# Kernel optimization log

Hardware: AMD Instinct MI355X
Metric: run time of the kernel (lower is better)

The kernel has to match this reference:

```python
import jax, jax.numpy as jnp
import numpy as np

S = 32          # input grid resolution
N = 2048        # active input voxels
C = 256         # in channels
CO = 128        # out channels
S2 = 2 * S      # upsampled resolution
M = 8 * N       # candidate child voxels
EPS = 1e-6


def setup_inputs() -> dict:
    key = jax.random.key(0)
    ks = jax.random.split(key, 8)
    # unique voxel coordinates (sparse occupancy)
    lin = jax.random.permutation(ks[0], S ** 3)[:N]
    coords = jnp.stack([lin // (S * S), (lin // S) % S, lin % S], axis=-1).astype(jnp.int32)
    sc = 0.05
    return {
        "feats": jax.random.normal(ks[1], (N, C), jnp.float32),
        "norm1_w": 1.0 + 0.1 * jax.random.normal(ks[2], (C,), jnp.float32),
        "norm1_b": 0.1 * jax.random.normal(ks[3], (C,), jnp.float32),
        "subdiv_w": sc * jax.random.normal(ks[4], (C, 8), jnp.float32),
        "subdiv_b": jnp.zeros((8,), jnp.float32),
        "conv1_w": sc * jax.random.normal(ks[5], (27, C, CO), jnp.float32),
        "conv1_b": jnp.zeros((CO,), jnp.float32),
        "conv2_w": sc * jax.random.normal(ks[6], (27, CO, CO), jnp.float32),
        "conv2_b": jnp.zeros((CO,), jnp.float32),
        "skip_w": sc * jax.random.normal(ks[7], (C, CO), jnp.float32),
        "skip_b": jnp.zeros((CO,), jnp.float32),
        "coords": coords,
    }


def _layernorm(x, w=None, b=None):
    # LayerNorm32: fp32 math, eps=1e-6
    m = jnp.mean(x, axis=-1, keepdims=True)
    v = jnp.var(x, axis=-1, keepdims=True)
    y = (x - m) * jax.lax.rsqrt(v + EPS)
    if w is not None:
        y = y * w + b
    return y


def _sparse_conv(feats, nidx, w, b):
    # submanifold 3x3x3 sparse conv: gather 27 neighbors, contract.
    # nidx: [M,27] with sentinel M pointing at a zero row.
    pad = jnp.concatenate([feats, jnp.zeros((1, feats.shape[1]), feats.dtype)], axis=0)
    g = pad[nidx]                                   # [M, 27, Cin]
    return jnp.einsum('nkc,kcd->nd', g, w) + b


def _forward(feats, norm1_w, norm1_b, subdiv_w, subdiv_b, conv1_w, conv1_b,
             conv2_w, conv2_b, skip_w, skip_b, coords):
    # subdiv prediction (SparseLinear C -> 8)
    subdiv = feats @ subdiv_w + subdiv_b            # [N, 8]
    # norm1 + silu
    h = jax.nn.silu(_layernorm(feats, norm1_w, norm1_b))
    # sparse upsample x2 with octree subdivision mask
    mask = (subdiv > 0).reshape(-1)                 # [M]
    j = jnp.arange(8, dtype=jnp.int32)
    offs8 = jnp.stack([(j >> 2) & 1, (j >> 1) & 1, j & 1], axis=-1)  # [8,3]
    cc = (coords[:, None, :] * 2 + offs8[None]).reshape(-1, 3)        # [M,3]
    h_c = jnp.where(mask[:, None], jnp.repeat(h, 8, axis=0), 0.0)     # [M,C]
    x_c = jnp.where(mask[:, None], jnp.repeat(feats, 8, axis=0), 0.0)
    # neighbor lookup grid (padded by 1; default M -> zero feature row)
    grid = jnp.full((S2 + 2, S2 + 2, S2 + 2), M, jnp.int32)
    grid = grid.at[cc[:, 0] + 1, cc[:, 1] + 1, cc[:, 2] + 1].set(
        jnp.arange(M, dtype=jnp.int32))
    d = jnp.arange(-1, 2, dtype=jnp.int32)
    offs27 = jnp.stack(jnp.meshgrid(d, d, d, indexing='ij'), axis=-1).reshape(27, 3)
    nc = cc[:, None, :] + 1 + offs27[None]          # [M,27,3]
    nidx = grid[nc[..., 0], nc[..., 1], nc[..., 2]] # [M,27]
    # conv1 -> norm2 (no affine) -> silu -> conv2
    h1 = jax.nn.silu(_layernorm(_sparse_conv(h_c, nidx, conv1_w, conv1_b)))
    h2 = _sparse_conv(h1, nidx, conv2_w, conv2_b)
    # residual with linear skip; mask out non-subdivided children
    out = (h2 + x_c @ skip_w + skip_b) * mask[:, None].astype(h2.dtype)
    return out, subdiv


def reference(feats, norm1_w, norm1_b, subdiv_w, subdiv_b, conv1_w, conv1_b,
              conv2_w, conv2_b, skip_w, skip_b, coords):
    return _forward(feats, norm1_w, norm1_b, subdiv_w, subdiv_b, conv1_w,
                    conv1_b, conv2_w, conv2_b, skip_w, skip_b, coords)
```

## Files before the change

kernel.cpp:

```cpp
#include <hip/hip_runtime.h>
#include <cstdint>
#include <cstddef>

constexpr int N  = 2048;
constexpr int C  = 256;
constexpr int CO = 128;
constexpr int M  = 16384;
constexpr int G  = 66;
constexpr int KP = 7;
constexpr int KCHUNK = 4;
constexpr float EPS = 1e-6f;

using bf8 = __attribute__((ext_vector_type(8))) short;
using f4  = __attribute__((ext_vector_type(4))) float;

#define AS1 __attribute__((address_space(1)))
#define AS3 __attribute__((address_space(3)))

static __device__ __forceinline__ void gl_lds16(const void* g, void* l) {
  __builtin_amdgcn_global_load_lds((AS1 const void*)g, (AS3 void*)l, 16, 0, 0);
}

static __device__ __forceinline__ unsigned short f2bf(float f) {
  unsigned u = __float_as_uint(f);
  u += 0x7fffu + ((u >> 16) & 1u);
  return (unsigned short)(u >> 16);
}

__global__ void k_init(int* __restrict__ grid, unsigned short* __restrict__ h,
                       unsigned short* __restrict__ h1) {
  int i = blockIdx.x * 256 + threadIdx.x;
  if (i < G * G * G) grid[i] = M;
  if (i < C)  h[(size_t)N * C + i] = 0;
  if (i < CO) h1[(size_t)M * CO + i] = 0;
}

template <int CIN>
__global__ void k_wt(const float* __restrict__ w, unsigned short* __restrict__ wt) {
  int i = blockIdx.x * 256 + threadIdx.x;
  if (i >= 27 * CIN * CO) return;
  int c = i % CIN;
  int rest = i / CIN;
  int o = rest % CO;
  int k = rest / CO;
  wt[i] = f2bf(w[((size_t)(k * CIN + c)) * CO + o]);
}

__global__ __launch_bounds__(256) void k_rownorm(
    const float* __restrict__ feats, const float* __restrict__ n1w,
    const float* __restrict__ n1b, const float* __restrict__ sdw,
    const float* __restrict__ sdb, float* __restrict__ out_subdiv,
    unsigned short* __restrict__ h, int* __restrict__ pidx,
    float* __restrict__ maskf) {
  int n = blockIdx.x, t = threadIdx.x;
  float x = feats[(size_t)n * C + t];
  float4 w0 = *(const float4*)(sdw + t * 8);
  float4 w1 = *(const float4*)(sdw + t * 8 + 4);
  float v[10] = {x * w0.x, x * w0.y, x * w0.z, x * w0.w,
                 x * w1.x, x * w1.y, x * w1.z, x * w1.w, x, x * x};
#pragma unroll
  for (int mk = 1; mk < 64; mk <<= 1) {
#pragma unroll
    for (int j = 0; j < 10; ++j) v[j] += __shfl_xor(v[j], mk, 64);
  }
  __shared__ float red[4][10];
  int wave = t >> 6, lane = t & 63;
  if (lane == 0) {
#pragma unroll
    for (int j = 0; j < 10; ++j) red[wave][j] = v[j];
  }
  __syncthreads();
  float sums[10];
#pragma unroll
  for (int j = 0; j < 10; ++j)
    sums[j] = red[0][j] + red[1][j] + red[2][j] + red[3][j];
  float mean = sums[8] / (float)C;
  float var  = sums[9] / (float)C - mean * mean;
  float rstd = rsqrtf(var + EPS);
  if (t < 8) {
    float sd = sums[t] + sdb[t];
    out_subdiv[(size_t)n * 8 + t] = sd;
    bool mk = sd > 0.f;
    pidx[n * 8 + t]  = mk ? n : N;
    maskf[n * 8 + t] = mk ? 1.f : 0.f;
  }
  float y  = (x - mean) * rstd * n1w[t] + n1b[t];
  float sl = y / (1.f + __expf(-y));
  h[(size_t)n * C + t] = f2bf(sl);
}

__global__ void k_scatter(const int* __restrict__ coords, int* __restrict__ grid) {
  int m = blockIdx.x * 256 + threadIdx.x;
  if (m >= M) return;
  int p = m >> 3, j = m & 7;
  int x = coords[p * 3 + 0] * 2 + ((j >> 2) & 1) + 1;
  int y = coords[p * 3 + 1] * 2 + ((j >> 1) & 1) + 1;
  int z = coords[p * 3 + 2] * 2 + (j & 1) + 1;
  grid[(x * G + y) * G + z] = m;
}

__global__ void k_nidx(const int* __restrict__ coords, const int* __restrict__ grid,
                       const int* __restrict__ pidx, int* __restrict__ nidxt,
                       int* __restrict__ g1t) {
  int idx = blockIdx.x * 256 + threadIdx.x;
  if (idx >= M * 27) return;
  int m = idx & (M - 1);
  int k = idx >> 14;
  int p = m >> 3, j = m & 7;
  int dx = k / 9 - 1;
  int dy = (k / 3) % 3 - 1;
  int dz = k % 3 - 1;
  int x = coords[p * 3 + 0] * 2 + ((j >> 2) & 1) + 1 + dx;
  int y = coords[p * 3 + 1] * 2 + ((j >> 1) & 1) + 1 + dy;
  int z = coords[p * 3 + 2] * 2 + (j & 1) + 1 + dz;
  int gv = grid[(x * G + y) * G + z];
  nidxt[idx] = gv;
  g1t[idx] = (gv == M) ? N : pidx[gv];
}

__global__ __launch_bounds__(256) void k_skip(const float* __restrict__ feats,
                                              const float* __restrict__ skw,
                                              const float* __restrict__ skb,
                                              float* __restrict__ s) {
  __shared__ float tile[32][36];
  int t = threadIdx.x;
  int rb = (blockIdx.x >> 1) * 32;
  int ob = (blockIdx.x & 1) * 64;
  int o = ob + (t & 63);
  int rg = (t >> 6) * 8;
  float acc[8] = {0, 0, 0, 0, 0, 0, 0, 0};
  for (int cb = 0; cb < C; cb += 32) {
    __syncthreads();
    int row = t >> 3, cc = (t & 7) * 4;
    *(float4*)&tile[row][cc] =
        *(const float4*)(feats + (size_t)(rb + row) * C + cb + cc);
    __syncthreads();
    for (int c = 0; c < 32; ++c) {
      float wv = skw[(size_t)(cb + c) * CO + o];
#pragma unroll
      for (int r = 0; r < 8; ++r) acc[r] += tile[rg + r][c] * wv;
    }
  }
  float bv = skb[o];
#pragma unroll
  for (int r = 0; r < 8; ++r) s[(size_t)(rb + rg + r) * CO + o] = acc[r] + bv;
}

template <int CIN, int NCB>
__global__ __launch_bounds__(256, 4) void k_conv(
    const unsigned short* __restrict__ src, const int* __restrict__ gt,
    const unsigned short* __restrict__ wt, float* __restrict__ part) {
  __shared__ unsigned short sA[2][128 * 32];
  __shared__ unsigned short sB[2][128 * 32];
  const int t = threadIdx.x;
  const int w = t >> 6, lane = t & 63;
  const int quad = lane >> 4, ln = lane & 15;
  const int m0 = blockIdx.x * 128;
  const int kpart = blockIdx.y;
  const int k0 = kpart * KCHUNK;
  const int nk = min(KCHUNK, 27 - k0);
  const int nstage = nk * NCB;
  const int rh = (w >> 1) * 64, ch = (w & 1) * 64;

  const int srow = lane >> 2;
  const int gchunk = (lane & 3) ^ ((lane >> 3) & 3);

  int ga[KCHUNK][2];
#pragma unroll
  for (int kk = 0; kk < KCHUNK; ++kk) {
#pragma unroll
    for (int rr = 0; rr < 2; ++rr) {
      ga[kk][rr] = (kk < nk)
          ? gt[(size_t)(k0 + kk) * M + m0 + rr * 64 + w * 16 + (lane >> 2)]
          : 0;
    }
  }
  (void)srow;

  auto stage = [&](int s, int buf) {
    const int kk = s / NCB;
    const int cb = s - kk * NCB;
    const int colbase = cb * 32 + gchunk * 8;
#pragma unroll
    for (int rr = 0; rr < 2; ++rr) {
      gl_lds16(src + (size_t)ga[kk][rr] * CIN + colbase,
               &sA[buf][(rr * 64 + w * 16) * 32]);
    }
#pragma unroll
    for (int rr = 0; rr < 2; ++rr) {
      const int corow = rr * 64 + w * 16 + (lane >> 2);
      gl_lds16(wt + ((size_t)(k0 + kk) * CO + corow) * CIN + colbase,
               &sB[buf][(rr * 64 + w * 16) * 32]);
    }
  };

  f4 acc[16];
  f4 zero = {0.f, 0.f, 0.f, 0.f};
#pragma unroll
  for (int i = 0; i < 16; ++i) acc[i] = zero;

  const int slot = quad ^ ((ln >> 1) & 3);

  stage(0, 0);
  for (int s = 0; s < nstage; ++s) {
    __syncthreads();
    if (s + 1 < nstage) stage(s + 1, (s + 1) & 1);
    const unsigned short* pa = sA[s & 1];
    const unsigned short* pb = sB[s & 1];
    bf8 av[4], bv[4];
#pragma unroll
    for (int ti = 0; ti < 4; ++ti) {
      int row = rh + ti * 16 + ln;
      av[ti] = *(const bf8*)(pa + row * 32 + slot * 8);
    }
#pragma unroll
    for (int tj = 0; tj < 4; ++tj) {
      int row = ch + tj * 16 + ln;
      bv[tj] = *(const bf8*)(pb + row * 32 + slot * 8);
    }
#pragma unroll
    for (int ti = 0; ti < 4; ++ti)
#pragma unroll
      for (int tj = 0; tj < 4; ++tj)
        acc[ti * 4 + tj] = __builtin_amdgcn_mfma_f32_16x16x32_bf16(
            av[ti], bv[tj], acc[ti * 4 + tj], 0, 0, 0);
  }

  float* pp = part + ((size_t)kpart * M + m0) * CO;
#pragma unroll
  for (int ti = 0; ti < 4; ++ti) {
    int mrow = rh + ti * 16 + quad * 4;
#pragma unroll
    for (int tj = 0; tj < 4; ++tj) {
      int co = ch + tj * 16 + ln;
#pragma unroll
      for (int rr = 0; rr < 4; ++rr)
        pp[(size_t)(mrow + rr) * CO + co] = acc[ti * 4 + tj][rr];
    }
  }
}

__global__ __launch_bounds__(256) void k_r1(const float* __restrict__ p,
                                            const float* __restrict__ bias,
                                            unsigned short* __restrict__ h1) {
  int wave = threadIdx.x >> 6, lane = threadIdx.x & 63;
  int m = blockIdx.x * 4 + wave;
  float v0 = bias[lane], v1 = bias[lane + 64];
#pragma unroll
  for (int q = 0; q < KP; ++q) {
    const float* pq = p + ((size_t)q * M + m) * CO;
    v0 += pq[lane];
    v1 += pq[lane + 64];
  }
  float sum = v0 + v1, sq = v0 * v0 + v1 * v1;
#pragma unroll
  for (int mk = 1; mk < 64; mk <<= 1) {
    sum += __shfl_xor(sum, mk, 64);
    sq  += __shfl_xor(sq, mk, 64);
  }
  float mean = sum / (float)CO;
  float var  = sq / (float)CO - mean * mean;
  float rstd = rsqrtf(var + EPS);
  float y0 = (v0 - mean) * rstd;
  float y1 = (v1 - mean) * rstd;
  float s0 = y0 / (1.f + __expf(-y0));
  float s1 = y1 / (1.f + __expf(-y1));
  h1[(size_t)m * CO + lane]      = f2bf(s0);
  h1[(size_t)m * CO + lane + 64] = f2bf(s1);
}

__global__ __launch_bounds__(256) void k_r2(const float* __restrict__ p,
                                            const float* __restrict__ bias,
                                            const float* __restrict__ sres,
                                            const float* __restrict__ maskf,
                                            float* __restrict__ out) {
  int i = blockIdx.x * 256 + threadIdx.x;
  int m = i >> 5;
  int o4 = (i & 31) * 4;
  float4 acc = *(const float4*)(bias + o4);
#pragma unroll
  for (int q = 0; q < KP; ++q) {
    float4 a = *(const float4*)(p + ((size_t)q * M + m) * CO + o4);
    acc.x += a.x; acc.y += a.y; acc.z += a.z; acc.w += a.w;
  }
  float4 s = *(const float4*)(sres + (size_t)(m >> 3) * CO + o4);
  float mk = maskf[m];
  float4 r;
  r.x = (acc.x + s.x) * mk;
  r.y = (acc.y + s.y) * mk;
  r.z = (acc.z + s.z) * mk;
  r.w = (acc.w + s.w) * mk;
  *(float4*)(out + (size_t)m * CO + o4) = r;
}

extern "C" void kernel_launch(void* const* d_in, const int* in_sizes, int n_in,
                              void* d_out, int out_size, void* d_ws, size_t ws_size,
                              hipStream_t stream) {
  const float* feats = (const float*)d_in[0];
  const float* n1w   = (const float*)d_in[1];
  const float* n1b   = (const float*)d_in[2];
  const float* sdw   = (const float*)d_in[3];
  const float* sdb   = (const float*)d_in[4];
  const float* c1w   = (const float*)d_in[5];
  const float* c1b   = (const float*)d_in[6];
  const float* c2w   = (const float*)d_in[7];
  const float* c2b   = (const float*)d_in[8];
  const float* skw   = (const float*)d_in[9];
  const float* skb   = (const float*)d_in[10];
  const int* coords  = (const int*)d_in[11];
  float* out = (float*)d_out;

  char* ws = (char*)d_ws;
  size_t off = 0;
  auto alloc = [&](size_t bytes) -> char* {
    char* p = ws + off;
    off += (bytes + 255) & ~(size_t)255;
    return p;
  };
  unsigned short* h    = (unsigned short*)alloc((size_t)(N + 1) * C * 2);
  unsigned short* h1   = (unsigned short*)alloc((size_t)(M + 1) * CO * 2);
  int*   grid  = (int*)alloc((size_t)G * G * G * 4);
  int*   nidxt = (int*)alloc((size_t)27 * M * 4);
  int*   g1t   = (int*)alloc((size_t)27 * M * 4);
  int*   pidx  = (int*)alloc((size_t)M * 4);
  float* maskf = (float*)alloc((size_t)M * 4);
  float* sres  = (float*)alloc((size_t)N * CO * 4);
  unsigned short* w1t = (unsigned short*)alloc((size_t)27 * CO * C * 2);
  unsigned short* w2t = (unsigned short*)alloc((size_t)27 * CO * CO * 2);
  float* pc = (float*)alloc((size_t)KP * M * CO * 4);

  k_init<<<(G * G * G + 255) / 256, 256, 0, stream>>>(grid, h, h1);
  k_wt<C><<<(27 * C * CO + 255) / 256, 256, 0, stream>>>(c1w, w1t);
  k_wt<CO><<<(27 * CO * CO + 255) / 256, 256, 0, stream>>>(c2w, w2t);
  k_rownorm<<<N, 256, 0, stream>>>(feats, n1w, n1b, sdw, sdb,
                                   out + (size_t)M * CO, h, pidx, maskf);
  k_scatter<<<(M + 255) / 256, 256, 0, stream>>>(coords, grid);
  k_nidx<<<(M * 27 + 255) / 256, 256, 0, stream>>>(coords, grid, pidx, nidxt, g1t);
  k_skip<<<128, 256, 0, stream>>>(feats, skw, skb, sres);

  k_conv<C, 8><<<dim3(M / 128, KP), 256, 0, stream>>>(h, g1t, w1t, pc);
  k_r1<<<M / 4, 256, 0, stream>>>(pc, c1b, h1);

  k_conv<CO, 4><<<dim3(M / 128, KP), 256, 0, stream>>>(h1, nidxt, w2t, pc);
  k_r2<<<M * CO / 4 / 256, 256, 0, stream>>>(pc, c2b, sres, maskf, out);
}
```

Baseline: 206.4 us.

## Store conv partials in bf16, stage tiles via registers, merge setup kernels

Three setup kernels (grid init and both weight transposes) become one, and the grid scatter is folded into the row-norm kernel, which cuts launch count. The split-K conv partial sums are now stored as bf16 instead of fp32, halving the partial-buffer write and reduction read traffic, at the cost of precision in the summed conv outputs. The conv kernel's direct global-to-LDS loads are replaced by register prefetch and explicit swizzled LDS stores placed after the MFMAs. Its occupancy hint drops from 4 to 3.

```diff
diff --git a/kernel.cpp b/kernel.cpp
--- a/kernel.cpp
+++ b/kernel.cpp
@@ -14,36 +14,37 @@
 using bf8 = __attribute__((ext_vector_type(8))) short;
 using f4  = __attribute__((ext_vector_type(4))) float;
 
-#define AS1 __attribute__((address_space(1)))
-#define AS3 __attribute__((address_space(3)))
-
-static __device__ __forceinline__ void gl_lds16(const void* g, void* l) {
-  __builtin_amdgcn_global_load_lds((AS1 const void*)g, (AS3 void*)l, 16, 0, 0);
-}
-
 static __device__ __forceinline__ unsigned short f2bf(float f) {
   unsigned u = __float_as_uint(f);
   u += 0x7fffu + ((u >> 16) & 1u);
   return (unsigned short)(u >> 16);
 }
-
-__global__ void k_init(int* __restrict__ grid, unsigned short* __restrict__ h,
-                       unsigned short* __restrict__ h1) {
+static __device__ __forceinline__ float bf2f(unsigned short s) {
+  return __uint_as_float((unsigned)s << 16);
+}
+
+__global__ void k_prep(int* __restrict__ grid, unsigned short* __restrict__ h,
+                       unsigned short* __restrict__ h1,
+                       const float* __restrict__ c1w, unsigned short* __restrict__ w1t,
+                       const float* __restrict__ c2w, unsigned short* __restrict__ w2t) {
   int i = blockIdx.x * 256 + threadIdx.x;
   if (i < G * G * G) grid[i] = M;
   if (i < C)  h[(size_t)N * C + i] = 0;
   if (i < CO) h1[(size_t)M * CO + i] = 0;
-}
-
-template <int CIN>
-__global__ void k_wt(const float* __restrict__ w, unsigned short* __restrict__ wt) {
-  int i = blockIdx.x * 256 + threadIdx.x;
-  if (i >= 27 * CIN * CO) return;
-  int c = i % CIN;
-  int rest = i / CIN;
-  int o = rest % CO;
-  int k = rest / CO;
-  wt[i] = f2bf(w[((size_t)(k * CIN + c)) * CO + o]);
+  if (i < 27 * C * CO) {
+    int c = i % C;
+    int rest = i / C;
+    int o = rest % CO;
+    int k = rest / CO;
+    w1t[i] = f2bf(c1w[((size_t)(k * C + c)) * CO + o]);
+  }
+  if (i < 27 * CO * CO) {
+    int c = i % CO;
+    int rest = i / CO;
+    int o = rest % CO;
+    int k = rest / CO;
+    w2t[i] = f2bf(c2w[((size_t)(k * CO + c)) * CO + o]);
+  }
 }
 
 __global__ __launch_bounds__(256) void k_rownorm(
@@ -51,7 +52,8 @@
     const float* __restrict__ n1b, const float* __restrict__ sdw,
     const float* __restrict__ sdb, float* __restrict__ out_subdiv,
     unsigned short* __restrict__ h, int* __restrict__ pidx,
-    float* __restrict__ maskf) {
+    float* __restrict__ maskf, const int* __restrict__ coords,
+    int* __restrict__ grid) {
   int n = blockIdx.x, t = threadIdx.x;
   float x = feats[(size_t)n * C + t];
   float4 w0 = *(const float4*)(sdw + t * 8);
@@ -83,20 +85,14 @@
     bool mk = sd > 0.f;
     pidx[n * 8 + t]  = mk ? n : N;
     maskf[n * 8 + t] = mk ? 1.f : 0.f;
+    int xx = coords[n * 3 + 0] * 2 + ((t >> 2) & 1) + 1;
+    int yy = coords[n * 3 + 1] * 2 + ((t >> 1) & 1) + 1;
+    int zz = coords[n * 3 + 2] * 2 + (t & 1) + 1;
+    grid[(xx * G + yy) * G + zz] = n * 8 + t;
   }
   float y  = (x - mean) * rstd * n1w[t] + n1b[t];
   float sl = y / (1.f + __expf(-y));
   h[(size_t)n * C + t] = f2bf(sl);
-}
-
-__global__ void k_scatter(const int* __restrict__ coords, int* __restrict__ grid) {
-  int m = blockIdx.x * 256 + threadIdx.x;
-  if (m >= M) return;
-  int p = m >> 3, j = m & 7;
-  int x = coords[p * 3 + 0] * 2 + ((j >> 2) & 1) + 1;
-  int y = coords[p * 3 + 1] * 2 + ((j >> 1) & 1) + 1;
-  int z = coords[p * 3 + 2] * 2 + (j & 1) + 1;
-  grid[(x * G + y) * G + z] = m;
 }
 
 __global__ void k_nidx(const int* __restrict__ coords, const int* __restrict__ grid,
@@ -147,9 +143,9 @@
 }
 
 template <int CIN, int NCB>
-__global__ __launch_bounds__(256, 4) void k_conv(
+__global__ __launch_bounds__(256, 3) void k_conv(
     const unsigned short* __restrict__ src, const int* __restrict__ gt,
-    const unsigned short* __restrict__ wt, float* __restrict__ part) {
+    const unsigned short* __restrict__ wt, unsigned short* __restrict__ part) {
   __shared__ unsigned short sA[2][128 * 32];
   __shared__ unsigned short sB[2][128 * 32];
   const int t = threadIdx.x;
@@ -162,36 +158,34 @@
   const int nstage = nk * NCB;
   const int rh = (w >> 1) * 64, ch = (w & 1) * 64;
 
-  const int srow = lane >> 2;
-  const int gchunk = (lane & 3) ^ ((lane >> 3) & 3);
-
-  int ga[KCHUNK][2];
-#pragma unroll
-  for (int kk = 0; kk < KCHUNK; ++kk) {
-#pragma unroll
-    for (int rr = 0; rr < 2; ++rr) {
-      ga[kk][rr] = (kk < nk)
-          ? gt[(size_t)(k0 + kk) * M + m0 + rr * 64 + w * 16 + (lane >> 2)]
-          : 0;
-    }
-  }
-  (void)srow;
-
-  auto stage = [&](int s, int buf) {
+  const int row2 = t >> 1;
+  const int c0 = (t & 1) * 2;
+  const int x3 = (row2 >> 1) & 3;
+  const int wsl0 = row2 * 32 + ((c0) ^ x3) * 8;
+  const int wsl1 = row2 * 32 + ((c0 + 1) ^ x3) * 8;
+
+  int ga[KCHUNK];
+#pragma unroll
+  for (int kk = 0; kk < KCHUNK; ++kk)
+    ga[kk] = (kk < nk) ? gt[(size_t)(k0 + kk) * M + m0 + row2] : 0;
+
+  bf8 ra0, ra1, rb0, rb1;
+  auto loadreg = [&](int s) {
     const int kk = s / NCB;
     const int cb = s - kk * NCB;
-    const int colbase = cb * 32 + gchunk * 8;
-#pragma unroll
-    for (int rr = 0; rr < 2; ++rr) {
-      gl_lds16(src + (size_t)ga[kk][rr] * CIN + colbase,
-               &sA[buf][(rr * 64 + w * 16) * 32]);
-    }
-#pragma unroll
-    for (int rr = 0; rr < 2; ++rr) {
-      const int corow = rr * 64 + w * 16 + (lane >> 2);
-      gl_lds16(wt + ((size_t)(k0 + kk) * CO + corow) * CIN + colbase,
-               &sB[buf][(rr * 64 + w * 16) * 32]);
-    }
+    const unsigned short* pa = src + (size_t)ga[kk] * CIN + cb * 32 + c0 * 8;
+    const unsigned short* pb =
+        wt + ((size_t)(k0 + kk) * CO + row2) * CIN + cb * 32 + c0 * 8;
+    ra0 = *(const bf8*)(pa);
+    ra1 = *(const bf8*)(pa + 8);
+    rb0 = *(const bf8*)(pb);
+    rb1 = *(const bf8*)(pb + 8);
+  };
+  auto writelds = [&](int buf) {
+    *(bf8*)(sA[buf] + wsl0) = ra0;
+    *(bf8*)(sA[buf] + wsl1) = ra1;
+    *(bf8*)(sB[buf] + wsl0) = rb0;
+    *(bf8*)(sB[buf] + wsl1) = rb1;
   };
 
   f4 acc[16];
@@ -199,34 +193,33 @@
 #pragma unroll
   for (int i = 0; i < 16; ++i) acc[i] = zero;
 
-  const int slot = quad ^ ((ln >> 1) & 3);
-
-  stage(0, 0);
+  const int slot = (quad ^ ((ln >> 1) & 3)) * 8;
+
+  loadreg(0);
+  writelds(0);
   for (int s = 0; s < nstage; ++s) {
+    const bool have = (s + 1 < nstage);
+    if (have) loadreg(s + 1);
     __syncthreads();
-    if (s + 1 < nstage) stage(s + 1, (s + 1) & 1);
     const unsigned short* pa = sA[s & 1];
     const unsigned short* pb = sB[s & 1];
     bf8 av[4], bv[4];
 #pragma unroll
-    for (int ti = 0; ti < 4; ++ti) {
-      int row = rh + ti * 16 + ln;
-      av[ti] = *(const bf8*)(pa + row * 32 + slot * 8);
-    }
-#pragma unroll
-    for (int tj = 0; tj < 4; ++tj) {
-      int row = ch + tj * 16 + ln;
-      bv[tj] = *(const bf8*)(pb + row * 32 + slot * 8);
-    }
+    for (int ti = 0; ti < 4; ++ti)
+      av[ti] = *(const bf8*)(pa + (rh + ti * 16 + ln) * 32 + slot);
+#pragma unroll
+    for (int tj = 0; tj < 4; ++tj)
+      bv[tj] = *(const bf8*)(pb + (ch + tj * 16 + ln) * 32 + slot);
 #pragma unroll
     for (int ti = 0; ti < 4; ++ti)
 #pragma unroll
       for (int tj = 0; tj < 4; ++tj)
         acc[ti * 4 + tj] = __builtin_amdgcn_mfma_f32_16x16x32_bf16(
             av[ti], bv[tj], acc[ti * 4 + tj], 0, 0, 0);
-  }
-
-  float* pp = part + ((size_t)kpart * M + m0) * CO;
+    if (have) writelds((s + 1) & 1);
+  }
+
+  unsigned short* pp = part + ((size_t)kpart * M + m0) * CO;
 #pragma unroll
   for (int ti = 0; ti < 4; ++ti) {
     int mrow = rh + ti * 16 + quad * 4;
@@ -235,12 +228,12 @@
       int co = ch + tj * 16 + ln;
 #pragma unroll
       for (int rr = 0; rr < 4; ++rr)
-        pp[(size_t)(mrow + rr) * CO + co] = acc[ti * 4 + tj][rr];
+        pp[(size_t)(mrow + rr) * CO + co] = f2bf(acc[ti * 4 + tj][rr]);
     }
   }
 }
 
-__global__ __launch_bounds__(256) void k_r1(const float* __restrict__ p,
+__global__ __launch_bounds__(256) void k_r1(const unsigned short* __restrict__ p,
                                             const float* __restrict__ bias,
                                             unsigned short* __restrict__ h1) {
   int wave = threadIdx.x >> 6, lane = threadIdx.x & 63;
@@ -248,9 +241,9 @@
   float v0 = bias[lane], v1 = bias[lane + 64];
 #pragma unroll
   for (int q = 0; q < KP; ++q) {
-    const float* pq = p + ((size_t)q * M + m) * CO;
-    v0 += pq[lane];
-    v1 += pq[lane + 64];
+    const unsigned short* pq = p + ((size_t)q * M + m) * CO;
+    v0 += bf2f(pq[lane]);
+    v1 += bf2f(pq[lane + 64]);
   }
   float sum = v0 + v1, sq = v0 * v0 + v1 * v1;
 #pragma unroll
@@ -269,7 +262,7 @@
   h1[(size_t)m * CO + lane + 64] = f2bf(s1);
 }
 
-__global__ __launch_bounds__(256) void k_r2(const float* __restrict__ p,
+__global__ __launch_bounds__(256) void k_r2(const unsigned short* __restrict__ p,
                                             const float* __restrict__ bias,
                                             const float* __restrict__ sres,
                                             const float* __restrict__ maskf,
@@ -280,8 +273,9 @@
   float4 acc = *(const float4*)(bias + o4);
 #pragma unroll
   for (int q = 0; q < KP; ++q) {
-    float4 a = *(const float4*)(p + ((size_t)q * M + m) * CO + o4);
-    acc.x += a.x; acc.y += a.y; acc.z += a.z; acc.w += a.w;
+    ushort4 a = *(const ushort4*)(p + ((size_t)q * M + m) * CO + o4);
+    acc.x += bf2f(a.x); acc.y += bf2f(a.y);
+    acc.z += bf2f(a.z); acc.w += bf2f(a.w);
   }
   float4 s = *(const float4*)(sres + (size_t)(m >> 3) * CO + o4);
   float mk = maskf[m];
@@ -327,14 +321,13 @@
   float* sres  = (float*)alloc((size_t)N * CO * 4);
   unsigned short* w1t = (unsigned short*)alloc((size_t)27 * CO * C * 2);
   unsigned short* w2t = (unsigned short*)alloc((size_t)27 * CO * CO * 2);
-  float* pc = (float*)alloc((size_t)KP * M * CO * 4);
-
-  k_init<<<(G * G * G + 255) / 256, 256, 0, stream>>>(grid, h, h1);
-  k_wt<C><<<(27 * C * CO + 255) / 256, 256, 0, stream>>>(c1w, w1t);
-  k_wt<CO><<<(27 * CO * CO + 255) / 256, 256, 0, stream>>>(c2w, w2t);
+  unsigned short* pc  = (unsigned short*)alloc((size_t)KP * M * CO * 2);
+
+  k_prep<<<(27 * C * CO + 255) / 256, 256, 0, stream>>>(grid, h, h1, c1w, w1t,
+                                                        c2w, w2t);
   k_rownorm<<<N, 256, 0, stream>>>(feats, n1w, n1b, sdw, sdb,
-                                   out + (size_t)M * CO, h, pidx, maskf);
-  k_scatter<<<(M + 255) / 256, 256, 0, stream>>>(coords, grid);
+                                   out + (size_t)M * CO, h, pidx, maskf,
+                                   coords, grid);
   k_nidx<<<(M * 27 + 255) / 256, 256, 0, stream>>>(coords, grid, pidx, nidxt, g1t);
   k_skip<<<128, 256, 0, stream>>>(feats, skw, skb, sres);
 
```

New measurement: 190.6 us. -7.6%, faster.
